# Kernel tuning notes

Hardware: AMD Instinct MI355X
Metric: run time of the kernel (lower is better)

## Reference

```python
import jax, jax.numpy as jnp
import numpy as np

B, T, C, FFN, N_LAYER, LAYER_ID = 4, 2048, 1024, 4096, 24, 1
EPS = 1e-5


def setup_inputs() -> dict:
    key = jax.random.key(0)
    ks = jax.random.split(key, 10)
    scale = 0.02

    def w(k, shape):
        return (jax.random.normal(k, shape, jnp.float32) * scale)

    # RWKV-4 init formulas for layer_id=1, n_layer=24 (learned params, init per source)
    r01 = LAYER_ID / (N_LAYER - 1)
    r10 = 1.0 - LAYER_ID / N_LAYER
    ddd = np.arange(C, dtype=np.float64) / C
    h = np.arange(C, dtype=np.float64)
    decay = -5.0 + 8.0 * (h / (C - 1)) ** (0.7 + 1.3 * r01)
    zigzag = np.array([(i + 1) % 3 - 1 for i in range(C)], dtype=np.float64) * 0.5
    tfirst = np.log(0.3) + zigzag

    return {
        "x": jax.random.normal(ks[0], (B, T, C), jnp.float32),
        "ln1_w": jnp.ones((C,), jnp.float32), "ln1_b": jnp.zeros((C,), jnp.float32),
        "ln2_w": jnp.ones((C,), jnp.float32), "ln2_b": jnp.zeros((C,), jnp.float32),
        "time_decay": jnp.asarray(decay, jnp.float32),
        "time_first": jnp.asarray(tfirst, jnp.float32),
        "tmk": jnp.asarray(ddd ** r10, jnp.float32),
        "tmv": jnp.asarray(ddd ** r10 + 0.3 * r01, jnp.float32),
        "tmr": jnp.asarray(ddd ** (0.5 * r10), jnp.float32),
        "att_kw": w(ks[1], (C, C)), "att_vw": w(ks[2], (C, C)),
        "att_rw": w(ks[3], (C, C)), "att_ow": w(ks[4], (C, C)),
        "f_tmk": jnp.asarray(ddd ** r10, jnp.float32),
        "f_tmr": jnp.asarray(ddd ** r10, jnp.float32),
        "f_kw": w(ks[5], (FFN, C)), "f_rw": w(ks[6], (C, C)), "f_vw": w(ks[7], (C, FFN)),
    }


def _ln(z, g, b):
    m = jnp.mean(z, axis=-1, keepdims=True)
    v = jnp.mean(jnp.square(z - m), axis=-1, keepdims=True)
    return (z - m) * jax.lax.rsqrt(v + EPS) * g + b


def _shift(z):  # token shift: prepend zero row along T, drop last
    return jnp.pad(z, ((0, 0), (1, 0), (0, 0)))[:, :-1]


def _wkv(time_decay, u, k, v):
    # Numerically-stable RWKV-4 WKV recurrence (log-space max trick).
    # k, v: [B, T, C]; time_decay, u: [C]
    w = -jnp.exp(time_decay)  # per-channel decay (negative)
    kt = jnp.moveaxis(k, 1, 0)  # [T, B, C]
    vt = jnp.moveaxis(v, 1, 0)
    aa = jnp.zeros_like(kt[0])
    bb = jnp.zeros_like(kt[0])
    pp = jnp.full_like(kt[0], -1e38)

    def step(carry, kv):
        aa, bb, pp = carry
        kk, vv = kv
        ww = u + kk
        p = jnp.maximum(pp, ww)
        e1 = jnp.exp(pp - p)
        e2 = jnp.exp(ww - p)
        out = (e1 * aa + e2 * vv) / (e1 * bb + e2)
        ww2 = pp + w
        p2 = jnp.maximum(ww2, kk)
        e1b = jnp.exp(ww2 - p2)
        e2b = jnp.exp(kk - p2)
        return (e1b * aa + e2b * vv, e1b * bb + e2b, p2), out

    _, out = jax.lax.scan(step, (aa, bb, pp), (kt, vt))
    return jnp.moveaxis(out, 0, 1)  # [B, T, C]


def reference(x, ln1_w, ln1_b, ln2_w, ln2_b, time_decay, time_first,
              tmk, tmv, tmr, att_kw, att_vw, att_rw, att_ow,
              f_tmk, f_tmr, f_kw, f_rw, f_vw):
    # --- RWKV_TimeMix (layer_id != 0; protectors are identity in fwd for finite vals) ---
    h = _ln(x, ln1_w, ln1_b)
    hx = _shift(h)
    xk = h * tmk + hx * (1.0 - tmk)
    xv = h * tmv + hx * (1.0 - tmv)
    xr = h * tmr + hx * (1.0 - tmr)
    k = jnp.einsum('btc,dc->btd', xk, att_kw)
    v = jnp.einsum('btc,dc->btd', xv, att_vw)
    sr = jax.nn.sigmoid(jnp.einsum('btc,dc->btd', xr, att_rw))
    rwkv = sr * _wkv(time_decay, time_first, k, v)
    x = x + jnp.einsum('btd,cd->btc', rwkv, att_ow)
    # --- RWKV_ChannelMix ---
    h = _ln(x, ln2_w, ln2_b)
    hx = _shift(h)
    xk = h * f_tmk + hx * (1.0 - f_tmk)
    xr = h * f_tmr + hx * (1.0 - f_tmr)
    kk = jnp.square(jax.nn.relu(jnp.einsum('btc,fc->btf', xk, f_kw)))
    kv = jnp.einsum('btf,cf->btc', kk, f_vw)
    x = x + jax.nn.sigmoid(jnp.einsum('btc,dc->btd', xr, f_rw)) * kv
    return x
```

## Files before the change

kernel.cpp:

```cpp
#include <hip/hip_runtime.h>
#include <cstdint>

#define C_DIM 1024
#define T_DIM 2048
#define B_DIM 4
#define FFN_DIM 4096
#define NROWS (B_DIM * T_DIM)
#define NELEM ((size_t)NROWS * C_DIM)
#define MB ((size_t)1 << 20)
#define NSEG 32
#define SEGL (T_DIM / NSEG)

typedef __bf16 bf16;
typedef __bf16 bf16x4 __attribute__((ext_vector_type(4)));
typedef __bf16 bf16x8 __attribute__((ext_vector_type(8)));
typedef float  floatx4 __attribute__((ext_vector_type(4)));

#define GLDS(g, l) __builtin_amdgcn_global_load_lds(                          \
    (const __attribute__((address_space(1))) void*)(g),                       \
    (__attribute__((address_space(3))) void*)(l), 16, 0, 0)

struct W7 {
    const float* s[7];
    bf16*        d[7];
    int          cum[8];
};

__global__ __launch_bounds__(256) void f2b7_kernel(W7 w)
{
    int id = blockIdx.x * 256 + threadIdx.x;
    int seg = 0;
#pragma unroll
    for (int j = 1; j < 7; ++j) if (id >= w.cum[j]) seg = j;
    int i = id - w.cum[seg];
    float4 v = ((const float4*)w.s[seg])[i];
    bf16x4 o = { (bf16)v.x, (bf16)v.y, (bf16)v.z, (bf16)v.w };
    ((bf16x4*)w.d[seg])[i] = o;
}

template<bool HASV>
__global__ __launch_bounds__(256) void lnmix_kernel(const float* __restrict__ x,
                                                    const float* __restrict__ g,
                                                    const float* __restrict__ b,
                                                    const float* __restrict__ mk,
                                                    const float* __restrict__ mv,
                                                    const float* __restrict__ mr,
                                                    bf16* __restrict__ xk,
                                                    bf16* __restrict__ xv,
                                                    bf16* __restrict__ xr)
{
    int row = blockIdx.x;
    int t   = row & (T_DIM - 1);
    int tid = threadIdx.x;
    size_t i4 = (size_t)row * 256 + tid;

    float4 v  = ((const float4*)x)[i4];
    float4 vp = make_float4(0.f, 0.f, 0.f, 0.f);
    if (t != 0) vp = ((const float4*)x)[i4 - 256];

    float s   = v.x + v.y + v.z + v.w;
    float s2  = v.x * v.x + v.y * v.y + v.z * v.z + v.w * v.w;
    float sp  = vp.x + vp.y + vp.z + vp.w;
    float sp2 = vp.x * vp.x + vp.y * vp.y + vp.z * vp.z + vp.w * vp.w;
    for (int off = 32; off > 0; off >>= 1) {
        s   += __shfl_down(s,   off);
        s2  += __shfl_down(s2,  off);
        sp  += __shfl_down(sp,  off);
        sp2 += __shfl_down(sp2, off);
    }
    __shared__ float red[16];
    int lane = tid & 63, wid = tid >> 6;
    if (lane == 0) { red[wid] = s; red[4 + wid] = s2; red[8 + wid] = sp; red[12 + wid] = sp2; }
    __syncthreads();
    s   = red[0] + red[1] + red[2] + red[3];
    s2  = red[4] + red[5] + red[6] + red[7];
    sp  = red[8] + red[9] + red[10] + red[11];
    sp2 = red[12] + red[13] + red[14] + red[15];

    float mean  = s * (1.0f / C_DIM);
    float inv   = rsqrtf(s2 * (1.0f / C_DIM) - mean * mean + 1e-5f);
    float meanp = sp * (1.0f / C_DIM);
    float invp  = rsqrtf(sp2 * (1.0f / C_DIM) - meanp * meanp + 1e-5f);

    float4 gv = ((const float4*)g)[tid];
    float4 bv = ((const float4*)b)[tid];
    float4 hv, hp;
    hv.x = (v.x - mean) * inv * gv.x + bv.x;
    hv.y = (v.y - mean) * inv * gv.y + bv.y;
    hv.z = (v.z - mean) * inv * gv.z + bv.z;
    hv.w = (v.w - mean) * inv * gv.w + bv.w;
    if (t != 0) {
        hp.x = (vp.x - meanp) * invp * gv.x + bv.x;
        hp.y = (vp.y - meanp) * invp * gv.y + bv.y;
        hp.z = (vp.z - meanp) * invp * gv.z + bv.z;
        hp.w = (vp.w - meanp) * invp * gv.w + bv.w;
    } else {
        hp = make_float4(0.f, 0.f, 0.f, 0.f);
    }

    float4 m1 = ((const float4*)mk)[tid];
    bf16x4 o;
    o.x = (bf16)(hp.x + m1.x * (hv.x - hp.x));
    o.y = (bf16)(hp.y + m1.y * (hv.y - hp.y));
    o.z = (bf16)(hp.z + m1.z * (hv.z - hp.z));
    o.w = (bf16)(hp.w + m1.w * (hv.w - hp.w));
    ((bf16x4*)xk)[i4] = o;

    if (HASV) {
        float4 m2 = ((const float4*)mv)[tid];
        o.x = (bf16)(hp.x + m2.x * (hv.x - hp.x));
        o.y = (bf16)(hp.y + m2.y * (hv.y - hp.y));
        o.z = (bf16)(hp.z + m2.z * (hv.z - hp.z));
        o.w = (bf16)(hp.w + m2.w * (hv.w - hp.w));
        ((bf16x4*)xv)[i4] = o;
    }

    float4 m3 = ((const float4*)mr)[tid];
    o.x = (bf16)(hp.x + m3.x * (hv.x - hp.x));
    o.y = (bf16)(hp.y + m3.y * (hv.y - hp.y));
    o.z = (bf16)(hp.z + m3.z * (hv.z - hp.z));
    o.w = (bf16)(hp.w + m3.w * (hv.w - hp.w));
    ((bf16x4*)xr)[i4] = o;
}

#define EPI_NONE 0
#define EPI_SIG 1
#define EPI_RELU2 2
#define EPI_ADD 3
#define EPI_SCALEADD 4

struct GemmArgs {
    const bf16* A;
    const bf16* W;
    void*       Y;
    const float* X2;
    const bf16*  S;
    int N, K, epi, outBf16;
};

__global__ __launch_bounds__(512) void gemm_p(GemmArgs pr)
{
    __shared__ unsigned short As[3 * 16384];
    __shared__ unsigned short Bs[3 * 8192];

    int tid = threadIdx.x;
    int lid = blockIdx.x;
    const bf16* PA = pr.A;
    const bf16* PW = pr.W;
    void*       PY = pr.Y;
    const float* PX2 = pr.X2;
    const bf16*  PS  = pr.S;
    int N = pr.N, K = pr.K;
    int epi = pr.epi, obf = pr.outBf16;

    int ntn = N >> 7;
    int m_t, n_t;
    if (ntn == 8) {
        int xcd = lid & 7, s = lid >> 3;
        n_t = s & 7;
        m_t = (xcd << 2) | (s >> 3);
    } else {
        int sq = lid >> 3;
        n_t = (lid & 7) * 4 + (sq & 3);
        m_t = sq >> 2;
    }
    int m0 = m_t * 256, n0 = n_t * 128;

    int wv = tid >> 6;
    int ln = tid & 63;

    int srow = wv * 16 + (ln >> 2);
    int qsw  = ((ln & 3) - ((srow >> 1) & 3)) & 3;
    const bf16* Ag = PA + (size_t)(m0 + srow) * K + qsw * 8;
    const bf16* Wg = PW + (size_t)(n0 + srow) * K + qsw * 8;
    size_t rowK128 = (size_t)128 * K;

    unsigned short* AsW = As + wv * 512;
    unsigned short* BsW = Bs + wv * 512;

    int wm = (wv & 3) * 64, wn = (wv >> 2) * 64;
    int ra0 = wm + (ln & 15);
    int rb0 = wn + (ln & 15);
    int qa  = ln >> 4;
    int abase = ra0 * 32 + (((qa + ((ra0 >> 1) & 3)) & 3) * 8);
    int bbase = rb0 * 32 + (((qa + ((rb0 >> 1) & 3)) & 3) * 8);

    floatx4 acc[4][4] = {};

#define STAGE_A(kt, bi)                                                       \
    do {                                                                      \
        const bf16* _a = Ag + (size_t)(kt) * 64;                              \
        unsigned short* _d = AsW + (bi) * 16384;                              \
        GLDS(_a,                _d);                         \
        GLDS(_a + rowK128,      _d + 4096);                  \
        GLDS(_a + 32,           _d + 8192);                  \
        GLDS(_a + rowK128 + 32, _d + 12288);                 \
    } while (0)
#define STAGE_B(kt, bi)                                                       \
    do {                                                                      \
        const bf16* _b = Wg + (size_t)(kt) * 64;                              \
        unsigned short* _d = BsW + (bi) * 8192;                               \
        GLDS(_b,      _d);                                          \
        GLDS(_b + 32, _d + 4096);                                   \
    } while (0)

#define MFMA16(a, b)                                                          \
    do {                                                                      \
        _Pragma("unroll")                                                     \
        for (int i = 0; i < 4; ++i)                                           \
            _Pragma("unroll")                                                 \
            for (int j = 0; j < 4; ++j)                                       \
                acc[i][j] = __builtin_amdgcn_mfma_f32_16x16x32_bf16(          \
                    a[i], b[j], acc[i][j], 0, 0, 0);                          \
    } while (0)

    int nt = K >> 6;

    STAGE_A(0, 0); STAGE_B(0, 0);
    STAGE_A(1, 1); STAGE_B(1, 1);

    int bi = 0, bi2 = 2;
    for (int t = 0; t < nt; ++t) {
        if (t < nt - 1) asm volatile("s_waitcnt vmcnt(6)" ::: "memory");
        else            asm volatile("s_waitcnt vmcnt(0)" ::: "memory");
        __builtin_amdgcn_s_barrier();
        __builtin_amdgcn_sched_barrier(0);

        const unsigned short* A0 = As + bi * 16384 + abase;
        const unsigned short* B0 = Bs + bi * 8192  + bbase;
        int dost = (t + 2 < nt);

        bf16x8 a[4], b[4];
#pragma unroll
        for (int i = 0; i < 4; ++i) a[i] = *(const bf16x8*)(A0 + i * 512);
#pragma unroll
        for (int j = 0; j < 4; ++j) b[j] = *(const bf16x8*)(B0 + j * 512);
        if (dost) STAGE_A(t + 2, bi2);
        asm volatile("s_waitcnt lgkmcnt(0)" ::: "memory");
        __builtin_amdgcn_sched_barrier(0);
        MFMA16(a, b);

#pragma unroll
        for (int i = 0; i < 4; ++i) a[i] = *(const bf16x8*)(A0 + 8192 + i * 512);
#pragma unroll
        for (int j = 0; j < 4; ++j) b[j] = *(const bf16x8*)(B0 + 4096 + j * 512);
        if (dost) STAGE_B(t + 2, bi2);
        asm volatile("s_waitcnt lgkmcnt(0)" ::: "memory");
        __builtin_amdgcn_sched_barrier(0);
        MFMA16(a, b);

        bi  = (bi  == 2) ? 0 : bi  + 1;
        bi2 = (bi2 == 2) ? 0 : bi2 + 1;
    }

#undef STAGE_A
#undef STAGE_B
#undef MFMA16

    int row0 = (ln >> 4) * 4;
    int colb = n0 + wn + (ln & 15);
#pragma unroll
    for (int i = 0; i < 4; ++i) {
        int gm = m0 + wm + i * 16 + row0;
#pragma unroll
        for (int j = 0; j < 4; ++j) {
            int gn = colb + j * 16;
#pragma unroll
            for (int r = 0; r < 4; ++r) {
                size_t idx = (size_t)(gm + r) * N + gn;
                float v = acc[i][j][r];
                if (epi == EPI_SIG)        v = 1.0f / (1.0f + __expf(-v));
                else if (epi == EPI_RELU2) { float t2 = fmaxf(v, 0.0f); v = t2 * t2; }
                else if (epi == EPI_ADD)   v = PX2[idx] + v;
                else if (epi == EPI_SCALEADD) v = PX2[idx] + (float)PS[idx] * v;
                if (obf) ((bf16*)PY)[idx] = (bf16)v;
                else     ((float*)PY)[idx] = v;
            }
        }
    }
}

__global__ __launch_bounds__(256) void wkv_seg(const float* __restrict__ k,
                                               const float* __restrict__ v,
                                               const float* __restrict__ decay,
                                               float* __restrict__ sa,
                                               float* __restrict__ sb,
                                               float* __restrict__ sp)
{
    int idx = blockIdx.x * 256 + threadIdx.x;
    int c   = idx & (C_DIM - 1);
    int bs  = idx >> 10;
    int seg = bs & (NSEG - 1);
    int b   = bs >> 5;
    float w = -__expf(decay[c]);
    size_t base = ((size_t)b * T_DIM + (size_t)seg * SEGL) * C_DIM + c;
    float aa = 0.f, bb = 0.f, pp = -1e38f;
    for (int t = 0; t < SEGL; ++t) {
        size_t off = base + (size_t)t * C_DIM;
        float kk = k[off], vv = v[off];
        float ww2 = pp + w;
        float p2  = fmaxf(ww2, kk);
        float e1  = __expf(ww2 - p2);
        float e2  = __expf(kk - p2);
        aa = e1 * aa + e2 * vv;
        bb = e1 * bb + e2;
        pp = p2;
    }
    sa[idx] = aa; sb[idx] = bb; sp[idx] = pp;
}

__global__ __launch_bounds__(256) void wkv_comb(const float* __restrict__ sa,
                                                const float* __restrict__ sb,
                                                const float* __restrict__ sp,
                                                const float* __restrict__ decay,
                                                float* __restrict__ ia,
                                                float* __restrict__ ib,
                                                float* __restrict__ ip)
{
    int idx = blockIdx.x * 256 + threadIdx.x;
    int c = idx & (C_DIM - 1);
    int b = idx >> 10;
    float wL = -__expf(decay[c]) * (float)SEGL;
    float aa = 0.f, bb = 0.f, pp = -1e38f;
    size_t base = (size_t)b * NSEG * C_DIM + c;
    for (int j = 0; j < NSEG; ++j) {
        size_t o = base + (size_t)j * C_DIM;
        ia[o] = aa; ib[o] = bb; ip[o] = pp;
        float a_s = sa[o], b_s = sb[o], p_s = sp[o];
        float pd = pp + wL;
        float pn = fmaxf(pd, p_s);
        float e1 = __expf(pd - pn);
        float e2 = __expf(p_s - pn);
        aa = e1 * aa + e2 * a_s;
        bb = e1 * bb + e2 * b_s;
        pp = pn;
    }
}

__global__ __launch_bounds__(256) void wkv_out(const float* __restrict__ k,
                                               const float* __restrict__ v,
                                               const bf16* __restrict__ sr,
                                               const float* __restrict__ decay,
                                               const float* __restrict__ first,
                                               const float* __restrict__ ia,
                                               const float* __restrict__ ib,
                                               const float* __restrict__ ip,
                                               bf16* __restrict__ out)
{
    int idx = blockIdx.x * 256 + threadIdx.x;
    int c   = idx & (C_DIM - 1);
    int bs  = idx >> 10;
    int seg = bs & (NSEG - 1);
    int b   = bs >> 5;
    float w = -__expf(decay[c]);
    float u = first[c];
    float aa = ia[idx], bb = ib[idx], pp = ip[idx];
    size_t base = ((size_t)b * T_DIM + (size_t)seg * SEGL) * C_DIM + c;
    for (int t = 0; t < SEGL; ++t) {
        size_t off = base + (size_t)t * C_DIM;
        float kk = k[off], vv = v[off];
        float ww = u + kk;
        float p  = fmaxf(pp, ww);
        float e1 = __expf(pp - p);
        float e2 = __expf(ww - p);
        float o  = (e1 * aa + e2 * vv) / (e1 * bb + e2);
        out[off] = (bf16)((float)sr[off] * o);
        float ww2 = pp + w;
        float p2  = fmaxf(ww2, kk);
        float e1b = __expf(ww2 - p2);
        float e2b = __expf(kk - p2);
        aa = e1b * aa + e2b * vv;
        bb = e1b * bb + e2b;
        pp = p2;
    }
}

extern "C" void kernel_launch(void* const* d_in, const int* in_sizes, int n_in,
                              void* d_out, int out_size, void* d_ws, size_t ws_size,
                              hipStream_t stream)
{
    const float* x          = (const float*)d_in[0];
    const float* ln1_w      = (const float*)d_in[1];
    const float* ln1_b      = (const float*)d_in[2];
    const float* ln2_w      = (const float*)d_in[3];
    const float* ln2_b      = (const float*)d_in[4];
    const float* time_decay = (const float*)d_in[5];
    const float* time_first = (const float*)d_in[6];
    const float* tmk        = (const float*)d_in[7];
    const float* tmv        = (const float*)d_in[8];
    const float* tmr        = (const float*)d_in[9];
    const float* att_kw     = (const float*)d_in[10];
    const float* att_vw     = (const float*)d_in[11];
    const float* att_rw     = (const float*)d_in[12];
    const float* att_ow     = (const float*)d_in[13];
    const float* f_tmk      = (const float*)d_in[14];
    const float* f_tmr      = (const float*)d_in[15];
    const float* f_kw       = (const float*)d_in[16];
    const float* f_rw       = (const float*)d_in[17];
    const float* f_vw       = (const float*)d_in[18];
    float* out = (float*)d_out;

    char* W8 = (char*)d_ws;
    bf16* kw_b  = (bf16*)(W8 + 0 * MB);
    bf16* vw_b  = (bf16*)(W8 + 2 * MB);
    bf16* rw_b  = (bf16*)(W8 + 4 * MB);
    bf16* ow_b  = (bf16*)(W8 + 6 * MB);
    bf16* fkw_b = (bf16*)(W8 + 8 * MB);
    bf16* frw_b = (bf16*)(W8 + 16 * MB);
    bf16* fvw_b = (bf16*)(W8 + 18 * MB);

    bf16*  xk_b   = (bf16*)(W8 + 26 * MB);
    bf16*  xv_b   = (bf16*)(W8 + 42 * MB);
    bf16*  xr_b   = (bf16*)(W8 + 58 * MB);
    bf16*  rwkv_b = xk_b;
    bf16*  xk2_b  = (bf16*)(W8 + 26 * MB);
    bf16*  xr2_b  = (bf16*)(W8 + 42 * MB);
    bf16*  sr2_b  = (bf16*)(W8 + 58 * MB);
    float* kbuf   = (float*)(W8 + 74 * MB);
    float* vbuf   = (float*)(W8 + 106 * MB);
    bf16*  srb_b  = (bf16*)(W8 + 138 * MB);
    bf16*  kk_b   = (bf16*)(W8 + 106 * MB);

    size_t KB512 = (size_t)512 * 1024;
    float* sc_a = (float*)(W8 + 170 * MB);
    float* sc_b = (float*)(W8 + 170 * MB + 1 * KB512);
    float* sc_p = (float*)(W8 + 170 * MB + 2 * KB512);
    float* in_a = (float*)(W8 + 170 * MB + 3 * KB512);
    float* in_b = (float*)(W8 + 170 * MB + 4 * KB512);
    float* in_p = (float*)(W8 + 170 * MB + 5 * KB512);

    int nC4 = C_DIM * C_DIM / 4, nF4 = FFN_DIM * C_DIM / 4;
    W7 w7;
    const float* srcs[7] = { att_kw, att_vw, att_rw, att_ow, f_kw, f_rw, f_vw };
    bf16*        dsts[7] = { kw_b, vw_b, rw_b, ow_b, fkw_b, frw_b, fvw_b };
    int          cnts[7] = { nC4, nC4, nC4, nC4, nF4, nC4, nF4 };
    int cum = 0;
    for (int i = 0; i < 7; ++i) { w7.s[i] = srcs[i]; w7.d[i] = dsts[i]; w7.cum[i] = cum; cum += cnts[i]; }
    w7.cum[7] = cum;
    f2b7_kernel<<<cum / 256, 256, 0, stream>>>(w7);

    int segGrid = B_DIM * NSEG * C_DIM / 256;

    auto launch = [&](const bf16* A, const bf16* W, void* Y, const float* X2,
                      const bf16* S, int N, int K, int epi, int obf) {
        GemmArgs p; p.A = A; p.W = W; p.Y = Y; p.X2 = X2; p.S = S;
        p.N = N; p.K = K; p.epi = epi; p.outBf16 = obf;
        int grid = (NROWS / 256) * (N / 128);
        gemm_p<<<grid, 512, 0, stream>>>(p);
    };

    lnmix_kernel<true><<<NROWS, 256, 0, stream>>>(x, ln1_w, ln1_b, tmk, tmv, tmr,
                                                  xk_b, xv_b, xr_b);
    launch(xk_b, kw_b, kbuf,  nullptr, nullptr, C_DIM, C_DIM, EPI_NONE, 0);
    launch(xv_b, vw_b, vbuf,  nullptr, nullptr, C_DIM, C_DIM, EPI_NONE, 0);
    launch(xr_b, rw_b, srb_b, nullptr, nullptr, C_DIM, C_DIM, EPI_SIG,  1);
    wkv_seg<<<segGrid, 256, 0, stream>>>(kbuf, vbuf, time_decay, sc_a, sc_b, sc_p);
    wkv_comb<<<B_DIM * C_DIM / 256, 256, 0, stream>>>(sc_a, sc_b, sc_p, time_decay, in_a, in_b, in_p);
    wkv_out<<<segGrid, 256, 0, stream>>>(kbuf, vbuf, srb_b, time_decay, time_first,
                                         in_a, in_b, in_p, rwkv_b);
    launch(rwkv_b, ow_b, out, x, nullptr, C_DIM, C_DIM, EPI_ADD, 0);

    lnmix_kernel<false><<<NROWS, 256, 0, stream>>>(out, ln2_w, ln2_b, f_tmk, nullptr, f_tmr,
                                                   xk2_b, nullptr, xr2_b);
    launch(xr2_b, frw_b, sr2_b, nullptr, nullptr, C_DIM,   C_DIM, EPI_SIG,   1);
    launch(xk2_b, fkw_b, kk_b,  nullptr, nullptr, FFN_DIM, C_DIM, EPI_RELU2, 1);
    launch(kk_b,  fvw_b, out,   out,     sr2_b,   C_DIM, FFN_DIM, EPI_SCALEADD, 0);
}
```

Before: 539.8 us.

## Split GEMM k-step into four phases with barriers and setprio around MFMA

```diff
diff --git a/kernel.cpp b/kernel.cpp
--- a/kernel.cpp
+++ b/kernel.cpp
@@ -204,15 +204,8 @@
         GLDS(_b + 32, _d + 4096);                                   \
     } while (0)
 
-#define MFMA16(a, b)                                                          \
-    do {                                                                      \
-        _Pragma("unroll")                                                     \
-        for (int i = 0; i < 4; ++i)                                           \
-            _Pragma("unroll")                                                 \
-            for (int j = 0; j < 4; ++j)                                       \
-                acc[i][j] = __builtin_amdgcn_mfma_f32_16x16x32_bf16(          \
-                    a[i], b[j], acc[i][j], 0, 0, 0);                          \
-    } while (0)
+#define MFMA1(ai, bj, i, j)                                                   \
+    acc[i][j] = __builtin_amdgcn_mfma_f32_16x16x32_bf16(ai, bj, acc[i][j], 0, 0, 0)
 
     int nt = K >> 6;
 
@@ -229,25 +222,64 @@
         const unsigned short* A0 = As + bi * 16384 + abase;
         const unsigned short* B0 = Bs + bi * 8192  + bbase;
         int dost = (t + 2 < nt);
-
-        bf16x8 a[4], b[4];
+        int tn   = dost ? (t + 2) : 0;
+        const bf16* a2 = Ag + (size_t)tn * 64;
+        const bf16* b2 = Wg + (size_t)tn * 64;
+        unsigned short* dA = AsW + bi2 * 16384;
+        unsigned short* dB = BsW + bi2 * 8192;
+
+        bf16x8 a[4], p, q;
+
 #pragma unroll
         for (int i = 0; i < 4; ++i) a[i] = *(const bf16x8*)(A0 + i * 512);
-#pragma unroll
-        for (int j = 0; j < 4; ++j) b[j] = *(const bf16x8*)(B0 + j * 512);
-        if (dost) STAGE_A(t + 2, bi2);
+        p = *(const bf16x8*)(B0);
+        q = *(const bf16x8*)(B0 + 512);
+        if (dost) { GLDS(a2, dA); GLDS(a2 + rowK128, dA + 4096); }
+        __builtin_amdgcn_s_barrier();
         asm volatile("s_waitcnt lgkmcnt(0)" ::: "memory");
         __builtin_amdgcn_sched_barrier(0);
-        MFMA16(a, b);
-
-#pragma unroll
-        for (int i = 0; i < 4; ++i) a[i] = *(const bf16x8*)(A0 + 8192 + i * 512);
-#pragma unroll
-        for (int j = 0; j < 4; ++j) b[j] = *(const bf16x8*)(B0 + 4096 + j * 512);
-        if (dost) STAGE_B(t + 2, bi2);
+        __builtin_amdgcn_s_setprio(1);
+#pragma unroll
+        for (int i = 0; i < 4; ++i) { MFMA1(a[i], p, i, 0); MFMA1(a[i], q, i, 1); }
+        __builtin_amdgcn_s_setprio(0);
+        __builtin_amdgcn_s_barrier();
+
+        p = *(const bf16x8*)(B0 + 1024);
+        q = *(const bf16x8*)(B0 + 1536);
+        if (dost) { GLDS(a2 + 32, dA + 8192); GLDS(a2 + rowK128 + 32, dA + 12288); }
+        __builtin_amdgcn_s_barrier();
         asm volatile("s_waitcnt lgkmcnt(0)" ::: "memory");
         __builtin_amdgcn_sched_barrier(0);
-        MFMA16(a, b);
+        __builtin_amdgcn_s_setprio(1);
+#pragma unroll
+        for (int i = 0; i < 4; ++i) { MFMA1(a[i], p, i, 2); MFMA1(a[i], q, i, 3); }
+        __builtin_amdgcn_s_setprio(0);
+        __builtin_amdgcn_s_barrier();
+
+#pragma unroll
+        for (int i = 0; i < 4; ++i) a[i] = *(const bf16x8*)(A0 + 8192 + i * 512);
+        p = *(const bf16x8*)(B0 + 4096);
+        q = *(const bf16x8*)(B0 + 4096 + 512);
+        if (dost) GLDS(b2, dB);
+        __builtin_amdgcn_s_barrier();
+        asm volatile("s_waitcnt lgkmcnt(0)" ::: "memory");
+        __builtin_amdgcn_sched_barrier(0);
+        __builtin_amdgcn_s_setprio(1);
+#pragma unroll
+        for (int i = 0; i < 4; ++i) { MFMA1(a[i], p, i, 0); MFMA1(a[i], q, i, 1); }
+        __builtin_amdgcn_s_setprio(0);
+        __builtin_amdgcn_s_barrier();
+
+        p = *(const bf16x8*)(B0 + 4096 + 1024);
+        q = *(const bf16x8*)(B0 + 4096 + 1536);
+        if (dost) GLDS(b2 + 32, dB + 4096);
+        __builtin_amdgcn_s_barrier();
+        asm volatile("s_waitcnt lgkmcnt(0)" ::: "memory");
+        __builtin_amdgcn_sched_barrier(0);
+        __builtin_amdgcn_s_setprio(1);
+#pragma unroll
+        for (int i = 0; i < 4; ++i) { MFMA1(a[i], p, i, 2); MFMA1(a[i], q, i, 3); }
+        __builtin_amdgcn_s_setprio(0);
 
         bi  = (bi  == 2) ? 0 : bi  + 1;
         bi2 = (bi2 == 2) ? 0 : bi2 + 1;
@@ -255,7 +287,7 @@
 
 #undef STAGE_A
 #undef STAGE_B
-#undef MFMA16
+#undef MFMA1
 
     int row0 = (ln >> 4) * 4;
     int colb = n0 + wn + (ln & 15);
```

After: 592.8 us. 1.1x slower.

## Add 256x256-tile GEMM kernel for the FFN key projection

Applied to the files above, without the earlier changes.

```diff
diff --git a/kernel.cpp b/kernel.cpp
--- a/kernel.cpp
+++ b/kernel.cpp
@@ -191,17 +191,17 @@
     do {                                                                      \
         const bf16* _a = Ag + (size_t)(kt) * 64;                              \
         unsigned short* _d = AsW + (bi) * 16384;                              \
-        GLDS(_a,                _d);                         \
-        GLDS(_a + rowK128,      _d + 4096);                  \
-        GLDS(_a + 32,           _d + 8192);                  \
-        GLDS(_a + rowK128 + 32, _d + 12288);                 \
+        GLDS(_a,                _d);                                          \
+        GLDS(_a + rowK128,      _d + 4096);                                   \
+        GLDS(_a + 32,           _d + 8192);                                   \
+        GLDS(_a + rowK128 + 32, _d + 12288);                                  \
     } while (0)
 #define STAGE_B(kt, bi)                                                       \
     do {                                                                      \
         const bf16* _b = Wg + (size_t)(kt) * 64;                              \
         unsigned short* _d = BsW + (bi) * 8192;                               \
-        GLDS(_b,      _d);                                          \
-        GLDS(_b + 32, _d + 4096);                                   \
+        GLDS(_b,      _d);                                                    \
+        GLDS(_b + 32, _d + 4096);                                             \
     } while (0)
 
 #define MFMA16(a, b)                                                          \
@@ -273,6 +273,119 @@
                 else if (epi == EPI_RELU2) { float t2 = fmaxf(v, 0.0f); v = t2 * t2; }
                 else if (epi == EPI_ADD)   v = PX2[idx] + v;
                 else if (epi == EPI_SCALEADD) v = PX2[idx] + (float)PS[idx] * v;
+                if (obf) ((bf16*)PY)[idx] = (bf16)v;
+                else     ((float*)PY)[idx] = v;
+            }
+        }
+    }
+}
+
+__global__ __launch_bounds__(512) void gemm_w(GemmArgs pr)
+{
+    __shared__ unsigned short As[2 * 16384];
+    __shared__ unsigned short Bs[2 * 16384];
+
+    int tid = threadIdx.x;
+    int lid = blockIdx.x;
+    const bf16* PA = pr.A;
+    const bf16* PW = pr.W;
+    void*       PY = pr.Y;
+    int N = pr.N, K = pr.K;
+    int epi = pr.epi, obf = pr.outBf16;
+
+    int sq  = lid >> 3;
+    int n_t = (lid & 7) * 2 + (sq & 1);
+    int m_t = sq >> 1;
+    int m0 = m_t * 256, n0 = n_t * 256;
+
+    int wv = tid >> 6;
+    int ln = tid & 63;
+
+    int srow = wv * 16 + (ln >> 2);
+    int qsw  = ((ln & 3) - ((srow >> 1) & 3)) & 3;
+    const bf16* Ag = PA + (size_t)(m0 + srow) * K + qsw * 8;
+    const bf16* Wg = PW + (size_t)(n0 + srow) * K + qsw * 8;
+    size_t rowK128 = (size_t)128 * K;
+
+    unsigned short* AsW = As + wv * 512;
+    unsigned short* BsW = Bs + wv * 512;
+
+    int wm = (wv >> 2) * 128, wn = (wv & 3) * 64;
+    int ra0 = wm + (ln & 15);
+    int rb0 = wn + (ln & 15);
+    int qa  = ln >> 4;
+    int abase = ra0 * 32 + (((qa + ((ra0 >> 1) & 3)) & 3) * 8);
+    int bbase = rb0 * 32 + (((qa + ((rb0 >> 1) & 3)) & 3) * 8);
+
+    floatx4 acc[8][4] = {};
+
+#define WSTAGE(kt, bi)                                                        \
+    do {                                                                      \
+        const bf16* _a = Ag + (size_t)(kt) * 64;                              \
+        const bf16* _b = Wg + (size_t)(kt) * 64;                              \
+        unsigned short* _dA = AsW + (bi) * 16384;                             \
+        unsigned short* _dB = BsW + (bi) * 16384;                             \
+        GLDS(_a,                _dA);                 \
+        GLDS(_a + rowK128,      _dA + 4096);          \
+        GLDS(_a + 32,           _dA + 8192);          \
+        GLDS(_a + rowK128 + 32, _dA + 12288);         \
+        GLDS(_b,                _dB);                                         \
+        GLDS(_b + rowK128,      _dB + 4096);                                  \
+        GLDS(_b + 32,           _dB + 8192);                                  \
+        GLDS(_b + rowK128 + 32, _dB + 12288);                                 \
+    } while (0)
+
+    int nt = K >> 6;
+
+    WSTAGE(0, 0);
+    asm volatile("s_waitcnt vmcnt(0)" ::: "memory");
+    __builtin_amdgcn_s_barrier();
+    __builtin_amdgcn_sched_barrier(0);
+
+    for (int t = 0; t < nt; ++t) {
+        int bi = t & 1;
+        if (t + 1 < nt) WSTAGE(t + 1, bi ^ 1);
+
+        const unsigned short* A0 = As + bi * 16384 + abase;
+        const unsigned short* B0 = Bs + bi * 16384 + bbase;
+
+#pragma unroll
+        for (int s = 0; s < 2; ++s) {
+            bf16x8 a[8], b[4];
+#pragma unroll
+            for (int i = 0; i < 8; ++i) a[i] = *(const bf16x8*)(A0 + s * 8192 + i * 512);
+#pragma unroll
+            for (int j = 0; j < 4; ++j) b[j] = *(const bf16x8*)(B0 + s * 8192 + j * 512);
+            asm volatile("s_waitcnt lgkmcnt(0)" ::: "memory");
+            __builtin_amdgcn_sched_barrier(0);
+#pragma unroll
+            for (int i = 0; i < 8; ++i)
+#pragma unroll
+                for (int j = 0; j < 4; ++j)
+                    acc[i][j] = __builtin_amdgcn_mfma_f32_16x16x32_bf16(
+                        a[i], b[j], acc[i][j], 0, 0, 0);
+        }
+
+        asm volatile("s_waitcnt vmcnt(0)" ::: "memory");
+        __builtin_amdgcn_s_barrier();
+        __builtin_amdgcn_sched_barrier(0);
+    }
+#undef WSTAGE
+
+    int row0 = (ln >> 4) * 4;
+    int colb = n0 + wn + (ln & 15);
+#pragma unroll
+    for (int i = 0; i < 8; ++i) {
+        int gm = m0 + wm + i * 16 + row0;
+#pragma unroll
+        for (int j = 0; j < 4; ++j) {
+            int gn = colb + j * 16;
+#pragma unroll
+            for (int r = 0; r < 4; ++r) {
+                size_t idx = (size_t)(gm + r) * N + gn;
+                float v = acc[i][j][r];
+                if (epi == EPI_RELU2) { float t2 = fmaxf(v, 0.0f); v = t2 * t2; }
+                else if (epi == EPI_SIG) v = 1.0f / (1.0f + __expf(-v));
                 if (obf) ((bf16*)PY)[idx] = (bf16)v;
                 else     ((float*)PY)[idx] = v;
             }
@@ -463,6 +576,10 @@
     lnmix_kernel<false><<<NROWS, 256, 0, stream>>>(out, ln2_w, ln2_b, f_tmk, nullptr, f_tmr,
                                                    xk2_b, nullptr, xr2_b);
     launch(xr2_b, frw_b, sr2_b, nullptr, nullptr, C_DIM,   C_DIM, EPI_SIG,   1);
-    launch(xk2_b, fkw_b, kk_b,  nullptr, nullptr, FFN_DIM, C_DIM, EPI_RELU2, 1);
+    {
+        GemmArgs p; p.A = xk2_b; p.W = fkw_b; p.Y = kk_b; p.X2 = nullptr; p.S = nullptr;
+        p.N = FFN_DIM; p.K = C_DIM; p.epi = EPI_RELU2; p.outBf16 = 1;
+        gemm_w<<<(NROWS / 256) * (FFN_DIM / 256), 512, 0, stream>>>(p);
+    }
     launch(kk_b,  fvw_b, out,   out,     sr2_b,   C_DIM, FFN_DIM, EPI_SCALEADD, 0);
 }
```

Result: faster. 528.7 us (-2.1%).
